# Kernel optimization log

Hardware: AMD Instinct MI355X
Metric: run time of the kernel (lower is better)

Reference implementation:

```python
import jax, jax.numpy as jnp
import numpy as np

N_NODES = 100000
N_EDGES = 1600000
D_FEAT = 128
UNITS = 128
LEAKY_ALPHA = 0.2  # tf.nn.leaky_relu default


def setup_inputs() -> dict:
    key = jax.random.key(0)
    k1, k2, k3, k4 = jax.random.split(key, 4)
    node_states = jax.random.normal(k1, (N_NODES, D_FEAT), dtype=jnp.float32)
    edges = jax.random.randint(k2, (N_EDGES, 2), 0, N_NODES, dtype=jnp.int64)
    kernel = jax.random.normal(k3, (D_FEAT, UNITS), dtype=jnp.float32) * (1.0 / np.sqrt(D_FEAT))
    kernel_attention = jax.random.normal(k4, (2 * UNITS, 1), dtype=jnp.float32) * (1.0 / np.sqrt(2 * UNITS))
    return {
        "node_states": node_states,
        "edges": edges,
        "kernel": kernel,
        "kernel_attention": kernel_attention,
    }


def reference(node_states, edges, kernel, kernel_attention):
    n = node_states.shape[0]
    tgt_idx = edges[:, 0]
    src_idx = edges[:, 1]

    # node_states_transformed: [N, units]
    h = node_states @ kernel

    # Attention logits. concat([tgt, src]) @ ka == tgt @ ka_t + src @ ka_s
    # (avoids materializing the [E, 2*units] concat).
    ka_t = kernel_attention[:UNITS, 0]   # [units]
    ka_s = kernel_attention[UNITS:, 0]   # [units]
    score_t = h @ ka_t                   # [N]
    score_s = h @ ka_s                   # [N]
    e = score_t[tgt_idx] + score_s[src_idx]              # [E]
    e = jax.nn.leaky_relu(e, negative_slope=LEAKY_ALPHA)
    e = jnp.exp(jnp.clip(e, -2.0, 2.0))

    # Segment softmax over incoming edges of each target node.
    sum_e = jax.ops.segment_sum(e, tgt_idx, num_segments=n)  # [N]
    attention = e / (sum_e[tgt_idx] + 1e-9)                  # [E]

    # Weighted scatter-sum of source messages.
    messages = h[src_idx] * attention[:, None]               # [E, units]
    output = jax.ops.segment_sum(messages, tgt_idx, num_segments=n)  # [N, units]
    return output
```

## Files before the change

### kernel.cpp

```cpp
#include <hip/hip_runtime.h>
#include <stdint.h>

typedef unsigned short ushort_t;
typedef __attribute__((ext_vector_type(8))) short short8;
typedef __attribute__((ext_vector_type(4))) float float4v;
typedef __attribute__((ext_vector_type(2))) float float2v;

#define N_NODES 100000
#define N_EDGES 1600000
#define D 128
#define NB_GEMM 1563
#define NBP     782
#define NB_B1   250
#define EPB     6400
#define BUCKETS 782
#define CAP     2560

static __device__ __forceinline__ float2v up2(uint32_t u) {
    float2v r;
    r.x = __builtin_bit_cast(float, u << 16);
    r.y = __builtin_bit_cast(float, u & 0xffff0000u);
    return r;
}
static __device__ __forceinline__ uint32_t f2bf_u(float f) {
    uint32_t u = __builtin_bit_cast(uint32_t, f);
    return (u + 0x7fffu + ((u >> 16) & 1u)) >> 16;
}
static __device__ __forceinline__ ushort_t f2bf(float f) {
    return (ushort_t)f2bf_u(f);
}
static __device__ __forceinline__ uint32_t pack2(float a, float b) {
    return f2bf_u(a) | (f2bf_u(b) << 16);
}
static __device__ __forceinline__ float edge_e(float s) {
    float x = (s >= 0.0f) ? s : 0.2f * s;
    x = fminf(fmaxf(x, -2.0f), 2.0f);
    return __expf(x);
}

__global__ void __launch_bounds__(256) prep_kernel(const float* __restrict__ W,
                                                   const float* __restrict__ KA,
                                                   float* __restrict__ wa,
                                                   ushort_t* __restrict__ WT,
                                                   const int* __restrict__ E,
                                                   int* __restrict__ eflag) {
    __shared__ int s;
    int b = blockIdx.x, t = threadIdx.x;
    int i = b * 256 + t;
    if (b < 64) {
        int k = i >> 7, nn = i & 127;
        int kb = k >> 5, q = (k >> 3) & 3, j = k & 7;
        int tt = nn >> 4, l = nn & 15;
        WT[((kb * 8 + tt) * 64 + q * 16 + l) * 8 + j] = f2bf(W[i]);
    } else if (b == 64) {
        if (t == 0) s = 0;
        __syncthreads();
        int nz = 0;
#pragma unroll
        for (int j = 0; j < 8; j++)
            if (E[(t + j * 256) * 2 + 1] != 0) nz = 1;
        if (nz) atomicOr(&s, 1);
        __syncthreads();
        if (t == 0) *eflag = (s == 0) ? 1 : 0;
    } else if (b == 65) {
        int half = t >> 7, k = t & 127;
        const float* kav = KA + half * 128;
        const float* wrow = W + k * 128;
        float acc = 0.0f;
#pragma unroll 8
        for (int j = 0; j < 128; j++) acc += wrow[j] * kav[j];
        wa[half * 128 + k] = acc;
    }
}

__global__ void __launch_bounds__(256) b1_kernel(const int* __restrict__ E,
                                                 const int* __restrict__ eflag,
                                                 int* __restrict__ sortedE,
                                                 ushort_t* __restrict__ bmat,
                                                 ushort_t* __restrict__ lofs) {
    __shared__ int lhist[1024];
    __shared__ int lpart[256];
    int eb = blockIdx.x, t = threadIdx.x;
    for (int j = t; j < 1024; j += 256) lhist[j] = 0;
    __syncthreads();
    int i64 = *eflag;
    int base = eb * EPB;
    int bin[25], w[25];
#pragma unroll
    for (int j = 0; j < 25; j++) {
        int i = base + j * 256 + t;
        int tgt, src;
        if (i64) { uint4 v = *(const uint4*)(E + (size_t)i * 4); tgt = (int)v.x; src = (int)v.z; }
        else     { uint2 v = *(const uint2*)(E + (size_t)i * 2); tgt = (int)v.x; src = (int)v.y; }
        if ((unsigned)tgt >= (unsigned)N_NODES) tgt = 0;
        if ((unsigned)src >= (unsigned)N_NODES) src = 0;
        bin[j] = tgt >> 7;
        w[j]   = ((tgt & 127) << 17) | src;
        atomicAdd(&lhist[bin[j]], 1);
    }
    __syncthreads();
    int c0 = lhist[t * 4], c1 = lhist[t * 4 + 1];
    int c2 = lhist[t * 4 + 2], c3 = lhist[t * 4 + 3];
    int sum = c0 + c1 + c2 + c3;
    lpart[t] = sum;
    __syncthreads();
    for (int off = 1; off < 256; off <<= 1) {
        int x = (t >= off) ? lpart[t - off] : 0;
        __syncthreads();
        lpart[t] += x;
        __syncthreads();
    }
    int e0 = lpart[t] - sum;
    int e1 = e0 + c0, e2 = e1 + c1, e3 = e2 + c2;
    int cc[4] = {c0, c1, c2, c3};
    int ee[4] = {e0, e1, e2, e3};
#pragma unroll
    for (int k = 0; k < 4; k++) {
        int bb = t * 4 + k;
        if (bb < BUCKETS) {
            bmat[eb * BUCKETS + bb] = (ushort_t)cc[k];
            lofs[eb * BUCKETS + bb] = (ushort_t)ee[k];
        }
    }
    lhist[t * 4] = e0; lhist[t * 4 + 1] = e1;
    lhist[t * 4 + 2] = e2; lhist[t * 4 + 3] = e3;
    __syncthreads();
#pragma unroll
    for (int j = 0; j < 25; j++) {
        int pos = atomicAdd(&lhist[bin[j]], 1);
        if (pos < EPB) sortedE[base + pos] = w[j];
    }
}

__global__ void __launch_bounds__(256) gemm_kernel(const float* __restrict__ X,
                                                   const ushort_t* __restrict__ WT,
                                                   const float* __restrict__ wa,
                                                   ushort_t* __restrict__ H,
                                                   float* __restrict__ st,
                                                   float* __restrict__ ss,
                                                   int M) {
    __shared__ ushort_t lds_wt[16384];
    int tid = threadIdx.x;
    {
        const uint4* srcp = (const uint4*)WT;
        uint4* dstp = (uint4*)lds_wt;
        for (int j = tid; j < 2048; j += 256) dstp[j] = srcp[j];
    }
    __syncthreads();

    int wave = tid >> 6, lane = tid & 63;
    int quad = lane >> 4, l16 = lane & 15;
    int t0 = blockIdx.x;
    int nt = (t0 + NBP < NB_GEMM) ? 2 : 1;

    float4 f[8];
    {
        int ar = t0 * 64 + wave * 16 + l16; if (ar >= M) ar = M - 1;
        const float* xr = X + (size_t)ar * D + quad * 8;
#pragma unroll
        for (int kb = 0; kb < 4; kb++) {
            f[kb * 2]     = *(const float4*)(xr + kb * 32);
            f[kb * 2 + 1] = *(const float4*)(xr + kb * 32 + 4);
        }
    }
    for (int it = 0; it < nt; it++) {
        int m0 = (t0 + it * NBP) * 64 + wave * 16;
        float4 nf[8];
        if (it + 1 < nt) {
            int ar = (t0 + NBP) * 64 + wave * 16 + l16; if (ar >= M) ar = M - 1;
            const float* xr = X + (size_t)ar * D + quad * 8;
#pragma unroll
            for (int kb = 0; kb < 4; kb++) {
                nf[kb * 2]     = *(const float4*)(xr + kb * 32);
                nf[kb * 2 + 1] = *(const float4*)(xr + kb * 32 + 4);
            }
        }
        short8 a[4];
        float sct = 0.0f, scs = 0.0f;
#pragma unroll
        for (int kb = 0; kb < 4; kb++) {
            float4 f0 = f[kb * 2], f1 = f[kb * 2 + 1];
            const float* wt0 = wa + kb * 32 + quad * 8;
            float4 t0v = *(const float4*)(wt0);
            float4 t1v = *(const float4*)(wt0 + 4);
            float4 s0v = *(const float4*)(wt0 + 128);
            float4 s1v = *(const float4*)(wt0 + 132);
            sct += f0.x * t0v.x + f0.y * t0v.y + f0.z * t0v.z + f0.w * t0v.w
                 + f1.x * t1v.x + f1.y * t1v.y + f1.z * t1v.z + f1.w * t1v.w;
            scs += f0.x * s0v.x + f0.y * s0v.y + f0.z * s0v.z + f0.w * s0v.w
                 + f1.x * s1v.x + f1.y * s1v.y + f1.z * s1v.z + f1.w * s1v.w;
            short8 v;
            v[0] = (short)f2bf(f0.x); v[1] = (short)f2bf(f0.y);
            v[2] = (short)f2bf(f0.z); v[3] = (short)f2bf(f0.w);
            v[4] = (short)f2bf(f1.x); v[5] = (short)f2bf(f1.y);
            v[6] = (short)f2bf(f1.z); v[7] = (short)f2bf(f1.w);
            a[kb] = v;
        }
        sct += __shfl_xor(sct, 16); sct += __shfl_xor(sct, 32);
        scs += __shfl_xor(scs, 16); scs += __shfl_xor(scs, 32);
        if (quad == 0 && m0 + l16 < M) { st[m0 + l16] = sct; ss[m0 + l16] = scs; }

        float4v acc[8] = {};
#pragma unroll
        for (int kb = 0; kb < 4; kb++) {
#pragma unroll
            for (int t = 0; t < 8; t++) {
                short8 b = *(const short8*)(&lds_wt[((kb * 8 + t) * 64 + lane) * 8]);
                acc[t] = __builtin_amdgcn_mfma_f32_16x16x32_bf16(a[kb], b, acc[t], 0, 0, 0);
            }
        }
#pragma unroll
        for (int r = 0; r < 4; r++) {
            int orow = m0 + quad * 4 + r;
            if (orow < M) {
                uint4 v;
                v.x = pack2(acc[0][r], acc[1][r]);
                v.y = pack2(acc[2][r], acc[3][r]);
                v.z = pack2(acc[4][r], acc[5][r]);
                v.w = pack2(acc[6][r], acc[7][r]);
                *(uint4*)(H + (size_t)orow * D + l16 * 8) = v;
            }
        }
        if (it + 1 < nt) {
#pragma unroll
            for (int j = 0; j < 8; j++) f[j] = nf[j];
        }
    }
}

__global__ void __launch_bounds__(512) agg2_kernel(const ushort_t* __restrict__ bmat,
                                                   const ushort_t* __restrict__ lofs,
                                                   const int* __restrict__ sortedE,
                                                   const float* __restrict__ st,
                                                   const float* __restrict__ ss,
                                                   const ushort_t* __restrict__ H,
                                                   float* __restrict__ out) {
    __shared__ int stage[CAP];
    __shared__ int sortedLoc[CAP];
    __shared__ int lh[128];
    __shared__ int lrp[129];
    __shared__ int wsum[8];
    __shared__ int lsoff[NB_B1];
    __shared__ int lsst[NB_B1];
    int b = blockIdx.x, t = threadIdx.x;
    int lane = t & 63, wv = t >> 6;
    int cnt = 0, sst = 0;
    if (t < NB_B1) {
        cnt = bmat[t * BUCKETS + b];
        sst = lofs[t * BUCKETS + b];
    }
    int x = cnt;
#pragma unroll
    for (int off = 1; off < 64; off <<= 1) {
        int y = __shfl_up(x, off);
        if (lane >= off) x += y;
    }
    if (lane == 63) wsum[wv] = x;
    if (t < 128) lh[t] = 0;
    __syncthreads();
    int wbase = 0, total = 0;
#pragma unroll
    for (int w = 0; w < 8; w++) {
        int sv = wsum[w];
        if (w < wv) wbase += sv;
        total += sv;
    }
    if (total > CAP) total = CAP;
    int soff = wbase + x - cnt;
    if (t < NB_B1) { lsoff[t] = soff; lsst[t] = sst; }
    __syncthreads();
    for (int j = t; j < total; j += 512) {
        int lo = 0, hi = NB_B1 - 1;
        while (lo < hi) {
            int mid = (lo + hi + 1) >> 1;
            if (lsoff[mid] <= j) lo = mid; else hi = mid - 1;
        }
        stage[j] = sortedE[lo * EPB + lsst[lo] + (j - lsoff[lo])];
    }
    __syncthreads();
    for (int j = t; j < total; j += 512)
        atomicAdd(&lh[stage[j] >> 17], 1);
    __syncthreads();
    int v = (t < 128) ? lh[t] : 0;
    int xs = v;
#pragma unroll
    for (int off = 1; off < 64; off <<= 1) {
        int y = __shfl_up(xs, off);
        if (lane >= off) xs += y;
    }
    if (t == 63) wsum[0] = xs;
    __syncthreads();
    if (t < 128) {
        int inc = (wv == 1) ? xs + wsum[0] : xs;
        int ex = inc - v;
        lrp[t] = ex;
        lh[t]  = ex;
    }
    if (t == 0) lrp[128] = total;
    __syncthreads();
    for (int j = t; j < total; j += 512) {
        int p = stage[j];
        int pos = atomicAdd(&lh[p >> 17], 1);
        if (pos < total) sortedLoc[pos] = p & 0x1FFFF;
    }
    __syncthreads();
    int g = lane >> 4, l = lane & 15;
    for (int nd = wv; nd < 128; nd += 8) {
        int gnode = b * 128 + nd;
        if (gnode >= N_NODES) break;
        int start = lrp[nd], end = lrp[nd + 1];
        float stn = st[gnode];
        float den = 0.0f;
        float2v acc2[4] = {};
        int m = start + g;
        for (; m + 12 < end; m += 16) {
            int s0 = sortedLoc[m],     s1 = sortedLoc[m + 4];
            int s2 = sortedLoc[m + 8], s3 = sortedLoc[m + 12];
            float e0 = edge_e(stn + ss[s0]);
            float e1 = edge_e(stn + ss[s1]);
            float e2 = edge_e(stn + ss[s2]);
            float e3 = edge_e(stn + ss[s3]);
            den += (e0 + e1) + (e2 + e3);
            uint4 p0 = *(const uint4*)(H + ((unsigned)s0 << 7) + l * 8);
            uint4 p1 = *(const uint4*)(H + ((unsigned)s1 << 7) + l * 8);
            uint4 p2 = *(const uint4*)(H + ((unsigned)s2 << 7) + l * 8);
            uint4 p3 = *(const uint4*)(H + ((unsigned)s3 << 7) + l * 8);
            float2v E0 = {e0, e0}, E1 = {e1, e1}, E2 = {e2, e2}, E3 = {e3, e3};
            acc2[0] += E0 * up2(p0.x) + E1 * up2(p1.x) + E2 * up2(p2.x) + E3 * up2(p3.x);
            acc2[1] += E0 * up2(p0.y) + E1 * up2(p1.y) + E2 * up2(p2.y) + E3 * up2(p3.y);
            acc2[2] += E0 * up2(p0.z) + E1 * up2(p1.z) + E2 * up2(p2.z) + E3 * up2(p3.z);
            acc2[3] += E0 * up2(p0.w) + E1 * up2(p1.w) + E2 * up2(p2.w) + E3 * up2(p3.w);
        }
        for (; m + 4 < end; m += 8) {
            int s0 = sortedLoc[m], s1 = sortedLoc[m + 4];
            float e0 = edge_e(stn + ss[s0]);
            float e1 = edge_e(stn + ss[s1]);
            den += e0 + e1;
            uint4 p0 = *(const uint4*)(H + ((unsigned)s0 << 7) + l * 8);
            uint4 p1 = *(const uint4*)(H + ((unsigned)s1 << 7) + l * 8);
            float2v E0 = {e0, e0}, E1 = {e1, e1};
            acc2[0] += E0 * up2(p0.x) + E1 * up2(p1.x);
            acc2[1] += E0 * up2(p0.y) + E1 * up2(p1.y);
            acc2[2] += E0 * up2(p0.z) + E1 * up2(p1.z);
            acc2[3] += E0 * up2(p0.w) + E1 * up2(p1.w);
        }
        if (m < end) {
            int s0 = sortedLoc[m];
            float e0 = edge_e(stn + ss[s0]);
            den += e0;
            uint4 p0 = *(const uint4*)(H + ((unsigned)s0 << 7) + l * 8);
            float2v E0 = {e0, e0};
            acc2[0] += E0 * up2(p0.x);
            acc2[1] += E0 * up2(p0.y);
            acc2[2] += E0 * up2(p0.z);
            acc2[3] += E0 * up2(p0.w);
        }
        den += __shfl_xor(den, 16);
        den += __shfl_xor(den, 32);
        float r[8];
#pragma unroll
        for (int j = 0; j < 4; j++) {
            float a0 = acc2[j].x, a1 = acc2[j].y;
            a0 += __shfl_xor(a0, 16); a0 += __shfl_xor(a0, 32);
            a1 += __shfl_xor(a1, 16); a1 += __shfl_xor(a1, 32);
            r[j * 2] = a0; r[j * 2 + 1] = a1;
        }
        float inv = 1.0f / (den + 1e-9f);
        if (g == 0) {
#pragma unroll
            for (int k = 0; k < 8; k++)
                out[(size_t)gnode * D + k * 16 + l] = r[k] * inv;
        }
    }
}

extern "C" void kernel_launch(void* const* d_in, const int* in_sizes, int n_in,
                              void* d_out, int out_size, void* d_ws, size_t ws_size,
                              hipStream_t stream) {
    const float* X  = (const float*)d_in[0];
    const int*   E  = (const int*)d_in[1];
    const float* W  = (const float*)d_in[2];
    const float* KA = (const float*)d_in[3];
    for (int i = 0; i < n_in; i++) {
        int s = in_sizes[i];
        if (s == N_NODES * D)      X  = (const float*)d_in[i];
        else if (s == N_EDGES * 2) E  = (const int*)d_in[i];
        else if (s == D * D)       W  = (const float*)d_in[i];
        else if (s == 2 * D)       KA = (const float*)d_in[i];
    }
    float* out = (float*)d_out;

    char* ws = (char*)d_ws;
    ushort_t* H        = (ushort_t*)(ws + 0);
    float*    wa       = (float*)   (ws + 25600000);
    float*    st       = (float*)   (ws + 25601024);
    float*    ssb      = (float*)   (ws + 26001024);
    int*      sortedE  = (int*)     (ws + 26401024);
    ushort_t* bmat     = (ushort_t*)(ws + 32801024);
    ushort_t* lofs     = (ushort_t*)(ws + 33192032);
    int*      eflag    = (int*)     (ws + 33583040);
    ushort_t* WT       = (ushort_t*)(ws + 33583072);

    prep_kernel<<<66, 256, 0, stream>>>(W, KA, wa, WT, E, eflag);
    b1_kernel<<<NB_B1, 256, 0, stream>>>(E, eflag, sortedE, bmat, lofs);
    gemm_kernel<<<NBP, 256, 0, stream>>>(X, WT, wa, H, st, ssb, N_NODES);
    agg2_kernel<<<BUCKETS, 512, 0, stream>>>(bmat, lofs, sortedE, st, ssb,
                                             H, out);
}
```

Before: 213.7 us.

## Fuse edge bucketing and GEMM into one launch, convert W to bf16 per block

Merges the edge-bucketing kernel and the node GEMM into a single launch: the first 521 blocks run the GEMM over three row tiles each, and the remaining 250 blocks do the edge histogram and sort. This removes one kernel launch and lets the two independent stages run on the GPU at the same time. Each GEMM block now converts and swizzles W from fp32 into bf16 in LDS itself, so prep no longer writes a WT buffer. The cost is redundant W conversion work in every GEMM block, and fewer GEMM blocks each doing more tiles.

```diff
diff --git a/kernel.cpp b/kernel.cpp
--- a/kernel.cpp
+++ b/kernel.cpp
@@ -10,7 +10,7 @@
 #define N_EDGES 1600000
 #define D 128
 #define NB_GEMM 1563
-#define NBP     782
+#define NBG     521
 #define NB_B1   250
 #define EPB     6400
 #define BUCKETS 782
@@ -41,18 +41,11 @@
 __global__ void __launch_bounds__(256) prep_kernel(const float* __restrict__ W,
                                                    const float* __restrict__ KA,
                                                    float* __restrict__ wa,
-                                                   ushort_t* __restrict__ WT,
                                                    const int* __restrict__ E,
                                                    int* __restrict__ eflag) {
     __shared__ int s;
     int b = blockIdx.x, t = threadIdx.x;
-    int i = b * 256 + t;
-    if (b < 64) {
-        int k = i >> 7, nn = i & 127;
-        int kb = k >> 5, q = (k >> 3) & 3, j = k & 7;
-        int tt = nn >> 4, l = nn & 15;
-        WT[((kb * 8 + tt) * 64 + q * 16 + l) * 8 + j] = f2bf(W[i]);
-    } else if (b == 64) {
+    if (b == 0) {
         if (t == 0) s = 0;
         __syncthreads();
         int nz = 0;
@@ -62,7 +55,7 @@
         if (nz) atomicOr(&s, 1);
         __syncthreads();
         if (t == 0) *eflag = (s == 0) ? 1 : 0;
-    } else if (b == 65) {
+    } else {
         int half = t >> 7, k = t & 127;
         const float* kav = KA + half * 128;
         const float* wrow = W + k * 128;
@@ -73,85 +66,97 @@
     }
 }
 
-__global__ void __launch_bounds__(256) b1_kernel(const int* __restrict__ E,
-                                                 const int* __restrict__ eflag,
-                                                 int* __restrict__ sortedE,
-                                                 ushort_t* __restrict__ bmat,
-                                                 ushort_t* __restrict__ lofs) {
-    __shared__ int lhist[1024];
-    __shared__ int lpart[256];
-    int eb = blockIdx.x, t = threadIdx.x;
-    for (int j = t; j < 1024; j += 256) lhist[j] = 0;
-    __syncthreads();
-    int i64 = *eflag;
-    int base = eb * EPB;
-    int bin[25], w[25];
-#pragma unroll
-    for (int j = 0; j < 25; j++) {
-        int i = base + j * 256 + t;
-        int tgt, src;
-        if (i64) { uint4 v = *(const uint4*)(E + (size_t)i * 4); tgt = (int)v.x; src = (int)v.z; }
-        else     { uint2 v = *(const uint2*)(E + (size_t)i * 2); tgt = (int)v.x; src = (int)v.y; }
-        if ((unsigned)tgt >= (unsigned)N_NODES) tgt = 0;
-        if ((unsigned)src >= (unsigned)N_NODES) src = 0;
-        bin[j] = tgt >> 7;
-        w[j]   = ((tgt & 127) << 17) | src;
-        atomicAdd(&lhist[bin[j]], 1);
-    }
-    __syncthreads();
-    int c0 = lhist[t * 4], c1 = lhist[t * 4 + 1];
-    int c2 = lhist[t * 4 + 2], c3 = lhist[t * 4 + 3];
-    int sum = c0 + c1 + c2 + c3;
-    lpart[t] = sum;
-    __syncthreads();
-    for (int off = 1; off < 256; off <<= 1) {
-        int x = (t >= off) ? lpart[t - off] : 0;
-        __syncthreads();
-        lpart[t] += x;
-        __syncthreads();
-    }
-    int e0 = lpart[t] - sum;
-    int e1 = e0 + c0, e2 = e1 + c1, e3 = e2 + c2;
-    int cc[4] = {c0, c1, c2, c3};
-    int ee[4] = {e0, e1, e2, e3};
-#pragma unroll
-    for (int k = 0; k < 4; k++) {
-        int bb = t * 4 + k;
-        if (bb < BUCKETS) {
-            bmat[eb * BUCKETS + bb] = (ushort_t)cc[k];
-            lofs[eb * BUCKETS + bb] = (ushort_t)ee[k];
-        }
-    }
-    lhist[t * 4] = e0; lhist[t * 4 + 1] = e1;
-    lhist[t * 4 + 2] = e2; lhist[t * 4 + 3] = e3;
-    __syncthreads();
-#pragma unroll
-    for (int j = 0; j < 25; j++) {
-        int pos = atomicAdd(&lhist[bin[j]], 1);
-        if (pos < EPB) sortedE[base + pos] = w[j];
-    }
-}
-
-__global__ void __launch_bounds__(256) gemm_kernel(const float* __restrict__ X,
-                                                   const ushort_t* __restrict__ WT,
-                                                   const float* __restrict__ wa,
-                                                   ushort_t* __restrict__ H,
-                                                   float* __restrict__ st,
-                                                   float* __restrict__ ss,
-                                                   int M) {
-    __shared__ ushort_t lds_wt[16384];
+__global__ void __launch_bounds__(256) fused_kernel(const float* __restrict__ X,
+                                                    const float* __restrict__ W,
+                                                    const float* __restrict__ wa,
+                                                    ushort_t* __restrict__ H,
+                                                    float* __restrict__ st,
+                                                    float* __restrict__ ss,
+                                                    int M,
+                                                    const int* __restrict__ E,
+                                                    const int* __restrict__ eflag,
+                                                    int* __restrict__ sortedE,
+                                                    ushort_t* __restrict__ bmat,
+                                                    ushort_t* __restrict__ lofs) {
+    __shared__ __align__(16) ushort_t lds_raw[16384];
     int tid = threadIdx.x;
+    if (blockIdx.x >= NBG) {
+        int eb = blockIdx.x - NBG;
+        int* lhist = (int*)lds_raw;
+        int* lpart = ((int*)lds_raw) + 1024;
+        int t = tid;
+        for (int j = t; j < 1024; j += 256) lhist[j] = 0;
+        __syncthreads();
+        int i64 = *eflag;
+        int base = eb * EPB;
+        int bin[25], w[25];
+#pragma unroll
+        for (int j = 0; j < 25; j++) {
+            int i = base + j * 256 + t;
+            int tgt, src;
+            if (i64) { uint4 v = *(const uint4*)(E + (size_t)i * 4); tgt = (int)v.x; src = (int)v.z; }
+            else     { uint2 v = *(const uint2*)(E + (size_t)i * 2); tgt = (int)v.x; src = (int)v.y; }
+            if ((unsigned)tgt >= (unsigned)N_NODES) tgt = 0;
+            if ((unsigned)src >= (unsigned)N_NODES) src = 0;
+            bin[j] = tgt >> 7;
+            w[j]   = ((tgt & 127) << 17) | src;
+            atomicAdd(&lhist[bin[j]], 1);
+        }
+        __syncthreads();
+        int c0 = lhist[t * 4], c1 = lhist[t * 4 + 1];
+        int c2 = lhist[t * 4 + 2], c3 = lhist[t * 4 + 3];
+        int sum = c0 + c1 + c2 + c3;
+        lpart[t] = sum;
+        __syncthreads();
+        for (int off = 1; off < 256; off <<= 1) {
+            int x = (t >= off) ? lpart[t - off] : 0;
+            __syncthreads();
+            lpart[t] += x;
+            __syncthreads();
+        }
+        int e0 = lpart[t] - sum;
+        int e1 = e0 + c0, e2 = e1 + c1, e3 = e2 + c2;
+        int cc[4] = {c0, c1, c2, c3};
+        int ee[4] = {e0, e1, e2, e3};
+#pragma unroll
+        for (int k = 0; k < 4; k++) {
+            int bb = t * 4 + k;
+            if (bb < BUCKETS) {
+                bmat[eb * BUCKETS + bb] = (ushort_t)cc[k];
+                lofs[eb * BUCKETS + bb] = (ushort_t)ee[k];
+            }
+        }
+        lhist[t * 4] = e0; lhist[t * 4 + 1] = e1;
+        lhist[t * 4 + 2] = e2; lhist[t * 4 + 3] = e3;
+        __syncthreads();
+#pragma unroll
+        for (int j = 0; j < 25; j++) {
+            int pos = atomicAdd(&lhist[bin[j]], 1);
+            if (pos < EPB) sortedE[base + pos] = w[j];
+        }
+        return;
+    }
     {
-        const uint4* srcp = (const uint4*)WT;
-        uint4* dstp = (uint4*)lds_wt;
-        for (int j = tid; j < 2048; j += 256) dstp[j] = srcp[j];
+        const float4* W4 = (const float4*)W;
+        for (int c = tid; c < 4096; c += 256) {
+            float4 w4 = W4[c];
+            int i0 = c * 4;
+            int k = i0 >> 7;
+            int kb = k >> 5, q = (k >> 3) & 3, jj = k & 7;
+            const float* wp = (const float*)&w4;
+#pragma unroll
+            for (int u = 0; u < 4; u++) {
+                int nn = (i0 + u) & 127;
+                int tt = nn >> 4, l = nn & 15;
+                lds_raw[((kb * 8 + tt) * 64 + q * 16 + l) * 8 + jj] = f2bf(wp[u]);
+            }
+        }
     }
     __syncthreads();
 
     int wave = tid >> 6, lane = tid & 63;
     int quad = lane >> 4, l16 = lane & 15;
     int t0 = blockIdx.x;
-    int nt = (t0 + NBP < NB_GEMM) ? 2 : 1;
 
     float4 f[8];
     {
@@ -163,11 +168,13 @@
             f[kb * 2 + 1] = *(const float4*)(xr + kb * 32 + 4);
         }
     }
-    for (int it = 0; it < nt; it++) {
-        int m0 = (t0 + it * NBP) * 64 + wave * 16;
+#pragma unroll
+    for (int it = 0; it < 3; it++) {
+        int m0 = (t0 + it * NBG) * 64 + wave * 16;
         float4 nf[8];
-        if (it + 1 < nt) {
-            int ar = (t0 + NBP) * 64 + wave * 16 + l16; if (ar >= M) ar = M - 1;
+        if (it < 2) {
+            int ar = (t0 + (it + 1) * NBG) * 64 + wave * 16 + l16;
+            if (ar >= M) ar = M - 1;
             const float* xr = X + (size_t)ar * D + quad * 8;
 #pragma unroll
             for (int kb = 0; kb < 4; kb++) {
@@ -205,7 +212,7 @@
         for (int kb = 0; kb < 4; kb++) {
 #pragma unroll
             for (int t = 0; t < 8; t++) {
-                short8 b = *(const short8*)(&lds_wt[((kb * 8 + t) * 64 + lane) * 8]);
+                short8 b = *(const short8*)(&lds_raw[((kb * 8 + t) * 64 + lane) * 8]);
                 acc[t] = __builtin_amdgcn_mfma_f32_16x16x32_bf16(a[kb], b, acc[t], 0, 0, 0);
             }
         }
@@ -221,7 +228,7 @@
                 *(uint4*)(H + (size_t)orow * D + l16 * 8) = v;
             }
         }
-        if (it + 1 < nt) {
+        if (it < 2) {
 #pragma unroll
             for (int j = 0; j < 8; j++) f[j] = nf[j];
         }
@@ -399,11 +406,11 @@
     ushort_t* bmat     = (ushort_t*)(ws + 32801024);
     ushort_t* lofs     = (ushort_t*)(ws + 33192032);
     int*      eflag    = (int*)     (ws + 33583040);
-    ushort_t* WT       = (ushort_t*)(ws + 33583072);
-
-    prep_kernel<<<66, 256, 0, stream>>>(W, KA, wa, WT, E, eflag);
-    b1_kernel<<<NB_B1, 256, 0, stream>>>(E, eflag, sortedE, bmat, lofs);
-    gemm_kernel<<<NBP, 256, 0, stream>>>(X, WT, wa, H, st, ssb, N_NODES);
+
+    prep_kernel<<<2, 256, 0, stream>>>(W, KA, wa, E, eflag);
+    fused_kernel<<<NBG + NB_B1, 256, 0, stream>>>(X, W, wa, H, st, ssb,
+                                                  N_NODES, E, eflag,
+                                                  sortedE, bmat, lofs);
     agg2_kernel<<<BUCKETS, 512, 0, stream>>>(bmat, lofs, sortedE, st, ssb,
                                              H, out);
 }
```

After: 215.3 us. Within noise of the previous version (+0.8%).
